# Performance work log

Measured on AMD Instinct MI355X. Metric: run time of the kernel, lower is better.

Reference implementation:

```python
import jax, jax.numpy as jnp
import numpy as np

DIM = 256
NUM_HEADS = 8
HEAD_DIM = DIM // NUM_HEADS


def _conv1x1(x, W, scale, bias):
    # 1x1 conv (bias=False) + eval-mode BN folded to per-channel scale/shift
    y = jnp.einsum('oc,bchw->bohw', W, x)
    return y * scale[None, :, None, None] + bias[None, :, None, None]


def setup_inputs() -> dict:
    key = jax.random.key(0)
    ks = jax.random.split(key, 16)
    B, H, W = 4, 64, 64
    Hu, Wu = 32, 32
    inp = {
        'x': jax.random.normal(ks[0], (B, DIM, H, W), jnp.float32),
        'upper_feat': jax.random.normal(ks[1], (B, DIM, Hu, Wu), jnp.float32),
        'Wq': jax.random.normal(ks[2], (DIM, DIM), jnp.float32) * 0.02,
        'q_scale': jax.random.uniform(ks[3], (DIM,), jnp.float32, 0.5, 1.5),
        'q_bias': jax.random.normal(ks[4], (DIM,), jnp.float32) * 0.02,
        'Wkv': jax.random.normal(ks[5], (2 * DIM, DIM), jnp.float32) * 0.02,
        'kv_scale': jax.random.uniform(ks[6], (2 * DIM,), jnp.float32, 0.5, 1.5),
        'kv_bias': jax.random.normal(ks[7], (2 * DIM,), jnp.float32) * 0.02,
        'Wpe': jax.random.normal(ks[8], (DIM, 1, 7, 7), jnp.float32) * 0.02,
        'pe_scale': jax.random.uniform(ks[9], (DIM,), jnp.float32, 0.5, 1.5),
        'pe_bias': jax.random.normal(ks[10], (DIM,), jnp.float32) * 0.02,
        'Wproj': jax.random.normal(ks[11], (DIM, DIM), jnp.float32) * 0.02,
        'proj_scale': jax.random.uniform(ks[12], (DIM,), jnp.float32, 0.5, 1.5),
        'proj_bias': jax.random.normal(ks[13], (DIM,), jnp.float32) * 0.02,
    }
    return inp


def reference(x, upper_feat, Wq, q_scale, q_bias, Wkv, kv_scale, kv_bias,
              Wpe, pe_scale, pe_bias, Wproj, proj_scale, proj_bias):
    B, C, H, W = x.shape
    N = H * W
    _, _, Hu, Wu = upper_feat.shape
    Nu = Hu * Wu

    # q branch: 1x1 conv+BN on x -> [B, heads, N, head_dim]
    q = _conv1x1(x, Wq, q_scale, q_bias)
    q = q.reshape(B, NUM_HEADS, HEAD_DIM, N).transpose(0, 1, 3, 2)

    # kv branch on upper (coarser) feature -> [B, heads, Nu, 2*head_dim]
    kv = _conv1x1(upper_feat, Wkv, kv_scale, kv_bias)
    kv = kv.reshape(B, NUM_HEADS, 2 * HEAD_DIM, Nu).transpose(0, 1, 3, 2)
    k, v = kv[..., :HEAD_DIM], kv[..., HEAD_DIM:]

    # cross attention: q over x pixels, k/v over upper pixels
    sim = jnp.einsum('bhnd,bhmd->bhnm', q, k) * (HEAD_DIM ** -0.5)
    attn = jax.nn.softmax(sim, axis=-1)
    ao = jnp.einsum('bhnm,bhmd->bhnd', attn, v)  # [B,h,N,hd]
    ao = ao.transpose(0, 1, 3, 2).reshape(B, C, H, W)

    # positional-encoding branch: depthwise 7x7 conv on v at upper resolution
    v_r = v.transpose(0, 1, 3, 2).reshape(B, C, Hu, Wu)
    v_pe = jax.lax.conv_general_dilated(
        v_r, Wpe, window_strides=(1, 1), padding=((3, 3), (3, 3)),
        feature_group_count=C,
        dimension_numbers=('NCHW', 'OIHW', 'NCHW'))
    v_pe = v_pe * pe_scale[None, :, None, None] + pe_bias[None, :, None, None]
    # bilinear upsample to x resolution (align_corners=False semantics)
    v_pe = jax.image.resize(v_pe, (B, C, H, W), method='bilinear')

    out = ao + v_pe
    return _conv1x1(out, Wproj, proj_scale, proj_bias)
```

## Files before the change

### kernel.cpp

```cpp
#include <hip/hip_runtime.h>
#include <hip/hip_bf16.h>

#define DIM 256
#define NHEADS 8
#define HDIM 32
#define Bq 4
#define Nq 4096
#define Nu 1024

typedef __attribute__((ext_vector_type(8))) short bf16x8;
typedef __attribute__((ext_vector_type(16))) float f32x16;
typedef __attribute__((ext_vector_type(4))) unsigned short us4;

__device__ __forceinline__ ushort f2bf(float x) {
    union { float f; unsigned u; } v; v.f = x;
    unsigned r = v.u + 0x7fffu + ((v.u >> 16) & 1u);
    return (ushort)(r >> 16);
}
__device__ __forceinline__ float bf2f(ushort u) {
    union { unsigned u; float f; } v; v.u = ((unsigned)u) << 16;
    return v.f;
}

__global__ __launch_bounds__(256) void prepro(
    const float* __restrict__ Wq, ushort* __restrict__ Oq,
    const float* __restrict__ Wkv, ushort* __restrict__ Okv,
    const float* __restrict__ Wp, ushort* __restrict__ Oph, ushort* __restrict__ Opl)
{
    const int i = blockIdx.x * 256 + threadIdx.x;
    if (i < 65536) {
        Oq[i] = f2bf(Wq[i]);
        float w = Wp[i];
        ushort h = f2bf(w);
        Oph[i] = h;
        Opl[i] = f2bf(w - bf2f(h));
    }
    Okv[i] = f2bf(Wkv[i]);
}

__global__ __launch_bounds__(256, 4) void qkv_mfma(
    const ushort* __restrict__ Wqb, const float* __restrict__ x,
    const float* __restrict__ q_scale, const float* __restrict__ q_bias, float qmult,
    const ushort* __restrict__ Wkvb, const float* __restrict__ upper,
    const float* __restrict__ kv_scale, const float* __restrict__ kv_bias,
    ushort* __restrict__ Qb, ushort* __restrict__ Kb, ushort* __restrict__ Vb)
{
    __shared__ __align__(16) ushort S[32 * 256];
    const int id = blockIdx.x;
    const int tid = threadIdx.x;

    const float* In; int N, n0, b, oh; bool isQ;
    if (id < 512) {
        isQ = true; In = x; N = 4096;
        n0 = (id & 127) * 32; b = id >> 7; oh = 0;
    } else {
        int q = id - 512;
        isQ = false; In = upper; N = 1024;
        n0 = (q & 31) * 32; oh = (q >> 5) & 1; b = q >> 6;
    }

    {
        const int n4 = (tid & 7) * 4, c8 = (tid >> 3) * 8;
        const float* ip = In + ((size_t)b * 256 + c8) * N + n0 + n4;
        unsigned ow[4][4];
        #pragma unroll
        for (int rp = 0; rp < 4; ++rp) {
            float4 f0 = *(const float4*)(ip + (size_t)(2 * rp) * N);
            float4 f1 = *(const float4*)(ip + (size_t)(2 * rp + 1) * N);
            asm("v_cvt_pk_bf16_f32 %0, %1, %2" : "=v"(ow[0][rp]) : "v"(f0.x), "v"(f1.x));
            asm("v_cvt_pk_bf16_f32 %0, %1, %2" : "=v"(ow[1][rp]) : "v"(f0.y), "v"(f1.y));
            asm("v_cvt_pk_bf16_f32 %0, %1, %2" : "=v"(ow[2][rp]) : "v"(f0.z), "v"(f1.z));
            asm("v_cvt_pk_bf16_f32 %0, %1, %2" : "=v"(ow[3][rp]) : "v"(f0.w), "v"(f1.w));
        }
        #pragma unroll
        for (int j = 0; j < 4; ++j) {
            const int n = n4 + j;
            const int slot = ((c8 >> 3) ^ (n & 15)) & 31;
            *(uint4*)(&S[n * 256 + (slot << 3)]) = *(const uint4*)&ow[j][0];
        }
    }
    __syncthreads();

    const int w = tid >> 6, l = tid & 63;
    const int l31 = l & 31, hi = l >> 5;
    const int nsw = l31 & 15;
    const ushort* Srow = &S[l31 * 256];

    if (isQ) {
        const ushort* w0 = Wqb + (size_t)(w * 64 + l31) * 256 + hi * 8;
        const ushort* w1 = w0 + (size_t)32 * 256;
        f32x16 acc0 = {}, acc1 = {};
        #pragma unroll 8
        for (int kk = 0; kk < 256; kk += 16) {
            const int slot = (((kk >> 3) + hi) ^ nsw) & 31;
            bf16x8 av = *(const bf16x8*)(Srow + (slot << 3));
            bf16x8 h0 = *(const bf16x8*)(w0 + kk);
            bf16x8 h1 = *(const bf16x8*)(w1 + kk);
            acc0 = __builtin_amdgcn_mfma_f32_32x32x16_bf16(av, h0, acc0, 0, 0, 0);
            acc1 = __builtin_amdgcn_mfma_f32_32x32x16_bf16(av, h1, acc1, 0, 0, 0);
        }
        #pragma unroll
        for (int t = 0; t < 2; ++t) {
            const f32x16 a = t ? acc1 : acc0;
            const int orow = w * 64 + t * 32 + l31;
            const float sc = q_scale[orow] * qmult;
            const float bi = q_bias[orow] * qmult;
            const int bh = b * 8 + 2 * w + t;
            ushort* Oa = Qb + ((size_t)bh * 4096) * 32 + l31;
            #pragma unroll
            for (int r = 0; r < 16; ++r) {
                const int dn = (r & 3) + 8 * (r >> 2) + 4 * hi;
                Oa[(size_t)(n0 + dn) * 32] = f2bf(a[r] * sc + bi);
            }
        }
    } else {
        const int h = oh * 4 + w;
        const ushort* wk = Wkvb + (size_t)(h * 64 + l31) * 256 + hi * 8;
        const ushort* wv = wk + (size_t)32 * 256;
        f32x16 accK = {}, accV = {};
        #pragma unroll 8
        for (int kk = 0; kk < 256; kk += 16) {
            const int slot = (((kk >> 3) + hi) ^ nsw) & 31;
            bf16x8 av = *(const bf16x8*)(Srow + (slot << 3));
            bf16x8 k0 = *(const bf16x8*)(wk + kk);
            bf16x8 v0 = *(const bf16x8*)(wv + kk);
            accK = __builtin_amdgcn_mfma_f32_32x32x16_bf16(av, k0, accK, 0, 0, 0);
            accV = __builtin_amdgcn_mfma_f32_32x32x16_bf16(v0, av, accV, 0, 0, 0);
        }
        const int bh = b * 8 + h;
        {
            const float sc = kv_scale[h * 64 + l31];
            const float bi = kv_bias[h * 64 + l31];
            ushort* Oa = Kb + ((size_t)bh * 1024) * 32 + l31;
            #pragma unroll
            for (int r = 0; r < 16; ++r) {
                const int dn = (r & 3) + 8 * (r >> 2) + 4 * hi;
                Oa[(size_t)(n0 + dn) * 32] = f2bf(accK[r] * sc + bi);
            }
        }
        {
            ushort* Ob = Vb + (size_t)bh * 32 * 1024;
            #pragma unroll
            for (int r = 0; r < 16; ++r) {
                const int dr = (r & 3) + 8 * (r >> 2) + 4 * hi;
                const float sc = kv_scale[h * 64 + 32 + dr];
                const float bi = kv_bias[h * 64 + 32 + dr];
                Ob[(size_t)dr * 1024 + n0 + l31] = f2bf(accV[r] * sc + bi);
            }
        }
    }
}

__global__ __launch_bounds__(256, 4) void attn_dw(
    const ushort* __restrict__ Qb, const ushort* __restrict__ Kt,
    const ushort* __restrict__ Vb, ushort* __restrict__ ao,
    const float* __restrict__ Wpe, const float* __restrict__ pe_scale,
    const float* __restrict__ pe_bias, ushort* __restrict__ vpe)
{
    __shared__ __align__(16) unsigned char smem[16384];
    const int tid = threadIdx.x;

    if (blockIdx.x < 1024) {
        const int w = tid >> 6, l = tid & 63;
        const int l31 = l & 31, hi = l >> 5;
        const int lid = blockIdx.x;
        const int j = lid >> 3;
        const int bh = (lid & 7) * 4 + (j >> 5);
        const int qbase = (j & 31) * 128 + w * 32;

        unsigned char (*ldsbuf)[8192] = (unsigned char(*)[8192])smem;

        const ushort* Qp = Qb + ((size_t)bh * 4096 + qbase) * 32;
        const unsigned char* Kg = (const unsigned char*)(Kt + (size_t)bh * 1024 * 32);
        const unsigned char* Vg = (const unsigned char*)(Vb + (size_t)bh * 32 * 1024);

        const bf16x8 qb0 = *(const bf16x8*)(Qp + (size_t)l31 * 32 + hi * 8);
        const bf16x8 qb1 = *(const bf16x8*)(Qp + (size_t)l31 * 32 + 16 + hi * 8);

        const int kr = tid >> 2, kc = tid & 3;
        const int vd = tid >> 3, vc = tid & 7;
        const int kwr = (kr * 64 + kc * 16) ^ ((kr & 7) << 4);
        const int vwr = vd * 128 + ((vc ^ (vd & 7)) << 4);

        f32x16 acc = {};
        float l_run = 0.f;

        uint4 kreg = *(const uint4*)(Kg + kr * 64 + kc * 16);
        uint4 vreg = *(const uint4*)(Vg + vd * 2048 + vc * 16);
        *(uint4*)(&ldsbuf[0][kwr]) = kreg;
        *(uint4*)(&ldsbuf[0][4096 + vwr]) = vreg;
        __syncthreads();

        for (int ph = 0; ph < 16; ++ph) {
            const int cur = ph & 1;
            if (ph < 15) {
                const size_t koff = (size_t)(ph + 1) * 4096;
                const int    voff = (ph + 1) * 128;
                kreg = *(const uint4*)(Kg + koff + kr * 64 + kc * 16);
                vreg = *(const uint4*)(Vg + (size_t)vd * 2048 + voff + vc * 16);
            }
            const unsigned char* Kl = &ldsbuf[cur][0];
            const unsigned char* Vl = &ldsbuf[cur][4096];

            #pragma unroll
            for (int s = 0; s < 2; ++s) {
                const int r = s * 32 + l31;
                bf16x8 ka0 = *(const bf16x8*)(Kl + ((r * 64 + hi * 16) ^ ((r & 7) << 4)));
                bf16x8 ka1 = *(const bf16x8*)(Kl + ((r * 64 + 32 + hi * 16) ^ ((r & 7) << 4)));
                bf16x8 va0 = *(const bf16x8*)(Vl + l31 * 128 + (((s * 4 + hi)     ^ (l31 & 7)) << 4));
                bf16x8 va1 = *(const bf16x8*)(Vl + l31 * 128 + (((s * 4 + 2 + hi) ^ (l31 & 7)) << 4));

                f32x16 sv = {};
                sv = __builtin_amdgcn_mfma_f32_32x32x16_bf16(ka0, qb0, sv, 0, 0, 0);
                sv = __builtin_amdgcn_mfma_f32_32x32x16_bf16(ka1, qb1, sv, 0, 0, 0);

                float p[16];
                #pragma unroll
                for (int r2 = 0; r2 < 16; ++r2) p[r2] = __builtin_amdgcn_exp2f(sv[r2]);
                l_run += (((p[0] + p[1]) + (p[2] + p[3])) + ((p[4] + p[5]) + (p[6] + p[7])))
                       + (((p[8] + p[9]) + (p[10] + p[11])) + ((p[12] + p[13]) + (p[14] + p[15])));

                int c[8];
                #pragma unroll
                for (int i = 0; i < 8; ++i)
                    asm("v_cvt_pk_bf16_f32 %0, %1, %2" : "=v"(c[i]) : "v"(p[2 * i]), "v"(p[2 * i + 1]));
                asm("v_permlane32_swap_b32 %0, %1" : "+v"(c[0]), "+v"(c[2]));
                asm("v_permlane32_swap_b32 %0, %1" : "+v"(c[1]), "+v"(c[3]));
                asm("v_permlane32_swap_b32 %0, %1" : "+v"(c[4]), "+v"(c[6]));
                asm("v_permlane32_swap_b32 %0, %1" : "+v"(c[5]), "+v"(c[7]));

                union { int i[4]; bf16x8 v; } b0u, b1u;
                b0u.i[0] = c[0]; b0u.i[1] = c[1]; b0u.i[2] = c[2]; b0u.i[3] = c[3];
                b1u.i[0] = c[4]; b1u.i[1] = c[5]; b1u.i[2] = c[6]; b1u.i[3] = c[7];

                acc = __builtin_amdgcn_mfma_f32_32x32x16_bf16(va0, b0u.v, acc, 0, 0, 0);
                acc = __builtin_amdgcn_mfma_f32_32x32x16_bf16(va1, b1u.v, acc, 0, 0, 0);
            }

            if (ph < 15) {
                const int nxt = cur ^ 1;
                *(uint4*)(&ldsbuf[nxt][kwr]) = kreg;
                *(uint4*)(&ldsbuf[nxt][4096 + vwr]) = vreg;
            }
            __syncthreads();
        }

        l_run += __shfl_xor(l_run, 32);
        float inv = 1.0f / l_run;

        ushort* aob = ao + ((size_t)(bh >> 3) * 256 + (bh & 7) * 32) * 4096 + qbase + l31;
        #pragma unroll
        for (int r = 0; r < 16; ++r) {
            const int d = (r & 3) + 8 * (r >> 2) + 4 * hi;
            aob[(size_t)d * 4096] = f2bf(acc[r] * inv);
        }
    } else {
        const int bc = blockIdx.x - 1024;
        const int b = bc >> 8, c = bc & 255;
        const ushort* vp = Vb + ((size_t)(b * 8 + (c >> 5)) * 32 + (c & 31)) * 1024;

        float* t   = (float*)smem;
        float* v32 = (float*)(smem + 5776);
        float* wl  = (float*)(smem + 9872);

        for (int i = tid; i < 38 * 38; i += 256) {
            int yy = i / 38 - 3, xx = i % 38 - 3;
            t[i] = (yy >= 0 && yy < 32 && xx >= 0 && xx < 32) ? bf2f(vp[yy * 32 + xx]) : 0.f;
        }
        if (tid < 49) wl[tid] = Wpe[(size_t)c * 49 + tid];
        __syncthreads();

        const float sc = pe_scale[c], bi = pe_bias[c];
        for (int i = tid; i < 1024; i += 256) {
            int y = i >> 5, x = i & 31;
            float s = 0.f;
            #pragma unroll
            for (int ky = 0; ky < 7; ++ky)
                #pragma unroll
                for (int kx = 0; kx < 7; ++kx)
                    s += t[(y + ky) * 38 + x + kx] * wl[ky * 7 + kx];
            v32[i] = s * sc + bi;
        }
        __syncthreads();

        ushort* op = vpe + (size_t)bc * 4096;
        #pragma unroll
        for (int p = 0; p < 16; ++p) {
            int idx = p * 256 + tid;
            int x = idx & 63, y = idx >> 6;
            float cx = x * 0.5f - 0.25f;
            float cy = y * 0.5f - 0.25f;
            int x0 = (x - 1) >> 1, y0 = (y - 1) >> 1;
            float fx = cx - x0, fy = cy - y0;
            int x0c = max(x0, 0), x1c = min(x0 + 1, 31);
            int y0c = max(y0, 0), y1c = min(y0 + 1, 31);
            float v00 = v32[y0c * 32 + x0c], v01 = v32[y0c * 32 + x1c];
            float v10 = v32[y1c * 32 + x0c], v11 = v32[y1c * 32 + x1c];
            float val = (1.f - fy) * ((1.f - fx) * v00 + fx * v01)
                      + fy * ((1.f - fx) * v10 + fx * v11);
            op[idx] = f2bf(val);
        }
    }
}

__global__ __launch_bounds__(512, 2) void proj_mfma(
    const ushort* __restrict__ Whi, const ushort* __restrict__ Wlo,
    const ushort* __restrict__ ao, const ushort* __restrict__ vpe,
    const float* __restrict__ scale, const float* __restrict__ bias,
    float* __restrict__ Out)
{
    __shared__ __align__(16) ushort S[64 * 256];
    const int tid = threadIdx.x;
    const int b  = blockIdx.z;
    const int n0 = blockIdx.x * 64;

    {
        const int n4 = (tid & 15) * 4;
        const int c8 = (tid >> 4) * 8;
        const ushort* ap = ao  + ((size_t)b * 256 + c8) * 4096 + n0 + n4;
        const ushort* vp = vpe + ((size_t)b * 256 + c8) * 4096 + n0 + n4;
        unsigned ow[4][4];
        #pragma unroll
        for (int rp = 0; rp < 4; ++rp) {
            uint2 a0 = *(const uint2*)(ap + (size_t)(2 * rp) * 4096);
            uint2 a1 = *(const uint2*)(ap + (size_t)(2 * rp + 1) * 4096);
            uint2 v0 = *(const uint2*)(vp + (size_t)(2 * rp) * 4096);
            uint2 v1 = *(const uint2*)(vp + (size_t)(2 * rp + 1) * 4096);
            const unsigned a0u[2] = { a0.x, a0.y };
            const unsigned a1u[2] = { a1.x, a1.y };
            const unsigned v0u[2] = { v0.x, v0.y };
            const unsigned v1u[2] = { v1.x, v1.y };
            #pragma unroll
            for (int q = 0; q < 2; ++q) {
                float s0lo = __uint_as_float(a0u[q] << 16)
                           + __uint_as_float(v0u[q] << 16);
                float s0hi = __uint_as_float(a0u[q] & 0xffff0000u)
                           + __uint_as_float(v0u[q] & 0xffff0000u);
                float s1lo = __uint_as_float(a1u[q] << 16)
                           + __uint_as_float(v1u[q] << 16);
                float s1hi = __uint_as_float(a1u[q] & 0xffff0000u)
                           + __uint_as_float(v1u[q] & 0xffff0000u);
                unsigned plo, phi;
                asm("v_cvt_pk_bf16_f32 %0, %1, %2" : "=v"(plo) : "v"(s0lo), "v"(s1lo));
                asm("v_cvt_pk_bf16_f32 %0, %1, %2" : "=v"(phi) : "v"(s0hi), "v"(s1hi));
                ow[2 * q][rp]     = plo;
                ow[2 * q + 1][rp] = phi;
            }
        }
        #pragma unroll
        for (int j = 0; j < 4; ++j) {
            const int n = n4 + j;
            const int slot = (((c8 >> 3) ^ (n & 15)) & 31);
            *(uint4*)(&S[n * 256 + (slot << 3)]) = *(const uint4*)&ow[j][0];
        }
    }
    __syncthreads();

    const int w = tid >> 6, l = tid & 63;
    const int l31 = l & 31, hi = l >> 5;
    const int wo = w & 3, wn = w >> 2;
    const int ob = wo * 64;

    const ushort* wh0 = Whi + (size_t)(ob + l31) * 256 + hi * 8;
    const ushort* wh1 = wh0 + (size_t)32 * 256;
    const ushort* wl0 = Wlo + (size_t)(ob + l31) * 256 + hi * 8;
    const ushort* wl1 = wl0 + (size_t)32 * 256;

    const int nloc = wn * 32 + l31;
    const ushort* Srow = &S[nloc * 256];
    const int nsw = nloc & 15;

    f32x16 acc0 = {}, acc1 = {};
    #pragma unroll 4
    for (int kk = 0; kk < 256; kk += 16) {
        const int slot = (((kk >> 3) + hi) ^ nsw) & 31;
        bf16x8 av = *(const bf16x8*)(Srow + (slot << 3));
        bf16x8 h0 = *(const bf16x8*)(wh0 + kk);
        bf16x8 h1 = *(const bf16x8*)(wh1 + kk);
        bf16x8 g0 = *(const bf16x8*)(wl0 + kk);
        bf16x8 g1 = *(const bf16x8*)(wl1 + kk);
        acc0 = __builtin_amdgcn_mfma_f32_32x32x16_bf16(h0, av, acc0, 0, 0, 0);
        acc1 = __builtin_amdgcn_mfma_f32_32x32x16_bf16(h1, av, acc1, 0, 0, 0);
        acc0 = __builtin_amdgcn_mfma_f32_32x32x16_bf16(g0, av, acc0, 0, 0, 0);
        acc1 = __builtin_amdgcn_mfma_f32_32x32x16_bf16(g1, av, acc1, 0, 0, 0);
    }

    float* Ob = Out + (size_t)b * 256 * 4096 + n0 + wn * 32 + l31;
    #pragma unroll
    for (int r = 0; r < 16; ++r) {
        const int dr = (r & 3) + 8 * (r >> 2) + 4 * hi;
        const int oA = ob + dr, oB = ob + 32 + dr;
        Ob[(size_t)oA * 4096] = acc0[r] * scale[oA] + bias[oA];
        Ob[(size_t)oB * 4096] = acc1[r] * scale[oB] + bias[oB];
    }
}

extern "C" void kernel_launch(void* const* d_in, const int* in_sizes, int n_in,
                              void* d_out, int out_size, void* d_ws, size_t ws_size,
                              hipStream_t stream)
{
    const float* x        = (const float*)d_in[0];
    const float* upper    = (const float*)d_in[1];
    const float* Wq       = (const float*)d_in[2];
    const float* q_scale  = (const float*)d_in[3];
    const float* q_bias   = (const float*)d_in[4];
    const float* Wkv      = (const float*)d_in[5];
    const float* kv_scale = (const float*)d_in[6];
    const float* kv_bias  = (const float*)d_in[7];
    const float* Wpe      = (const float*)d_in[8];
    const float* pe_scale = (const float*)d_in[9];
    const float* pe_bias  = (const float*)d_in[10];
    const float* Wproj    = (const float*)d_in[11];
    const float* proj_scale = (const float*)d_in[12];
    const float* proj_bias  = (const float*)d_in[13];
    float* out = (float*)d_out;

    ushort* Qb   = (ushort*)d_ws;
    ushort* Kb   = Qb + (size_t)32 * 4096 * 32;
    ushort* Vb   = Kb + (size_t)32 * 1024 * 32;
    ushort* ao   = Vb + (size_t)32 * 1024 * 32;
    ushort* vpe  = ao + (size_t)Bq * DIM * Nq;
    ushort* Wqb  = vpe + (size_t)Bq * DIM * Nq;
    ushort* Wkvb = Wqb + 256 * 256;
    ushort* Wph  = Wkvb + 512 * 256;
    ushort* Wpl  = Wph + 256 * 256;

    const float qmult = 0.17677669529663687f * 1.4426950408889634f;

    prepro<<<dim3(512), 256, 0, stream>>>(Wq, Wqb, Wkv, Wkvb, Wproj, Wph, Wpl);

    qkv_mfma<<<dim3(768), 256, 0, stream>>>(Wqb, x, q_scale, q_bias, qmult,
                                            Wkvb, upper, kv_scale, kv_bias,
                                            Qb, Kb, Vb);

    attn_dw<<<dim3(2048), 256, 0, stream>>>(Qb, Kb, Vb, ao,
                                            Wpe, pe_scale, pe_bias, vpe);

    proj_mfma<<<dim3(64, 1, 4), 512, 0, stream>>>(Wph, Wpl, ao, vpe,
                                                  proj_scale, proj_bias, out);
}
```

Before: 81.78 us.

## Fuse bilinear upsample of positional encoding into projection kernel prologue

The depthwise conv branch now writes the low-resolution fp32 result (32x32 per channel) to global memory, and the bilinear 2x upsample is done inside the projection kernel while it stages its input tile. This avoids writing and rereading a full-resolution bf16 vpe tensor. The projection prologue gains extra gather loads and arithmetic, with neighbouring pixels reread from L2, and the added value is no longer rounded to bf16 before summation.

```diff
diff --git a/kernel.cpp b/kernel.cpp
--- a/kernel.cpp
+++ b/kernel.cpp
@@ -19,6 +19,10 @@
 }
 __device__ __forceinline__ float bf2f(ushort u) {
     union { unsigned u; float f; } v; v.u = ((unsigned)u) << 16;
+    return v.f;
+}
+__device__ __forceinline__ float bfu2f(unsigned lo16shifted) {
+    union { unsigned u; float f; } v; v.u = lo16shifted;
     return v.f;
 }
 
@@ -155,7 +159,7 @@
     const ushort* __restrict__ Qb, const ushort* __restrict__ Kt,
     const ushort* __restrict__ Vb, ushort* __restrict__ ao,
     const float* __restrict__ Wpe, const float* __restrict__ pe_scale,
-    const float* __restrict__ pe_bias, ushort* __restrict__ vpe)
+    const float* __restrict__ pe_bias, float* __restrict__ v32f)
 {
     __shared__ __align__(16) unsigned char smem[16384];
     const int tid = threadIdx.x;
@@ -259,9 +263,8 @@
         const int b = bc >> 8, c = bc & 255;
         const ushort* vp = Vb + ((size_t)(b * 8 + (c >> 5)) * 32 + (c & 31)) * 1024;
 
-        float* t   = (float*)smem;
-        float* v32 = (float*)(smem + 5776);
-        float* wl  = (float*)(smem + 9872);
+        float* t  = (float*)smem;
+        float* wl = (float*)(smem + 5776);
 
         for (int i = tid; i < 38 * 38; i += 256) {
             int yy = i / 38 - 3, xx = i % 38 - 3;
@@ -271,6 +274,7 @@
         __syncthreads();
 
         const float sc = pe_scale[c], bi = pe_bias[c];
+        float* op = v32f + (size_t)bc * 1024;
         for (int i = tid; i < 1024; i += 256) {
             int y = i >> 5, x = i & 31;
             float s = 0.f;
@@ -279,79 +283,82 @@
                 #pragma unroll
                 for (int kx = 0; kx < 7; ++kx)
                     s += t[(y + ky) * 38 + x + kx] * wl[ky * 7 + kx];
-            v32[i] = s * sc + bi;
-        }
-        __syncthreads();
-
-        ushort* op = vpe + (size_t)bc * 4096;
-        #pragma unroll
-        for (int p = 0; p < 16; ++p) {
-            int idx = p * 256 + tid;
-            int x = idx & 63, y = idx >> 6;
-            float cx = x * 0.5f - 0.25f;
-            float cy = y * 0.5f - 0.25f;
-            int x0 = (x - 1) >> 1, y0 = (y - 1) >> 1;
-            float fx = cx - x0, fy = cy - y0;
-            int x0c = max(x0, 0), x1c = min(x0 + 1, 31);
-            int y0c = max(y0, 0), y1c = min(y0 + 1, 31);
-            float v00 = v32[y0c * 32 + x0c], v01 = v32[y0c * 32 + x1c];
-            float v10 = v32[y1c * 32 + x0c], v11 = v32[y1c * 32 + x1c];
-            float val = (1.f - fy) * ((1.f - fx) * v00 + fx * v01)
-                      + fy * ((1.f - fx) * v10 + fx * v11);
-            op[idx] = f2bf(val);
+            op[i] = s * sc + bi;
         }
     }
 }
 
 __global__ __launch_bounds__(512, 2) void proj_mfma(
     const ushort* __restrict__ Whi, const ushort* __restrict__ Wlo,
-    const ushort* __restrict__ ao, const ushort* __restrict__ vpe,
+    const ushort* __restrict__ ao, const float* __restrict__ v32f,
     const float* __restrict__ scale, const float* __restrict__ bias,
     float* __restrict__ Out)
 {
     __shared__ __align__(16) ushort S[64 * 256];
     const int tid = threadIdx.x;
     const int b  = blockIdx.z;
-    const int n0 = blockIdx.x * 64;
+    const int y  = blockIdx.x;
+    const int n0 = y * 64;
 
     {
-        const int n4 = (tid & 15) * 4;
+        const int m  = tid & 15;
         const int c8 = (tid >> 4) * 8;
-        const ushort* ap = ao  + ((size_t)b * 256 + c8) * 4096 + n0 + n4;
-        const ushort* vp = vpe + ((size_t)b * 256 + c8) * 4096 + n0 + n4;
-        unsigned ow[4][4];
-        #pragma unroll
-        for (int rp = 0; rp < 4; ++rp) {
-            uint2 a0 = *(const uint2*)(ap + (size_t)(2 * rp) * 4096);
-            uint2 a1 = *(const uint2*)(ap + (size_t)(2 * rp + 1) * 4096);
-            uint2 v0 = *(const uint2*)(vp + (size_t)(2 * rp) * 4096);
-            uint2 v1 = *(const uint2*)(vp + (size_t)(2 * rp + 1) * 4096);
-            const unsigned a0u[2] = { a0.x, a0.y };
-            const unsigned a1u[2] = { a1.x, a1.y };
-            const unsigned v0u[2] = { v0.x, v0.y };
-            const unsigned v1u[2] = { v1.x, v1.y };
-            #pragma unroll
-            for (int q = 0; q < 2; ++q) {
-                float s0lo = __uint_as_float(a0u[q] << 16)
-                           + __uint_as_float(v0u[q] << 16);
-                float s0hi = __uint_as_float(a0u[q] & 0xffff0000u)
-                           + __uint_as_float(v0u[q] & 0xffff0000u);
-                float s1lo = __uint_as_float(a1u[q] << 16)
-                           + __uint_as_float(v1u[q] << 16);
-                float s1hi = __uint_as_float(a1u[q] & 0xffff0000u)
-                           + __uint_as_float(v1u[q] & 0xffff0000u);
-                unsigned plo, phi;
-                asm("v_cvt_pk_bf16_f32 %0, %1, %2" : "=v"(plo) : "v"(s0lo), "v"(s1lo));
-                asm("v_cvt_pk_bf16_f32 %0, %1, %2" : "=v"(phi) : "v"(s0hi), "v"(s1hi));
-                ow[2 * q][rp]     = plo;
-                ow[2 * q + 1][rp] = phi;
-            }
-        }
+
+        const int y0  = (y - 1) >> 1;
+        const float fy = (y & 1) ? 0.25f : 0.75f;
+        const float gy = 1.0f - fy;
+        const int y0c = max(y0, 0), y1c = min(y0 + 1, 31);
+        const int aIdx = max(m - 1, 0), cIdx = min(m + 1, 15);
+
+        float sval[4][8];
+        #pragma unroll
+        for (int cc = 0; cc < 8; ++cc) {
+            const int ch = c8 + cc;
+            const float* rowb = v32f + (size_t)(b * 256 + ch) * 1024;
+            const float* rT = rowb + y0c * 32;
+            const float* rB = rowb + y1c * 32;
+            float2 ta = *(const float2*)(rT + 2 * aIdx);
+            float2 tb = *(const float2*)(rT + 2 * m);
+            float2 tc = *(const float2*)(rT + 2 * cIdx);
+            float2 ba = *(const float2*)(rB + 2 * aIdx);
+            float2 bb = *(const float2*)(rB + 2 * m);
+            float2 bc2 = *(const float2*)(rB + 2 * cIdx);
+            const float t_m1 = (m == 0)  ? tb.x : ta.y;
+            const float t_p2 = (m == 15) ? tb.y : tc.x;
+            const float b_m1 = (m == 0)  ? bb.x : ba.y;
+            const float b_p2 = (m == 15) ? bb.y : bc2.x;
+            const float ht0 = 0.25f * t_m1 + 0.75f * tb.x;
+            const float ht1 = 0.75f * tb.x + 0.25f * tb.y;
+            const float ht2 = 0.25f * tb.x + 0.75f * tb.y;
+            const float ht3 = 0.75f * tb.y + 0.25f * t_p2;
+            const float hb0 = 0.25f * b_m1 + 0.75f * bb.x;
+            const float hb1 = 0.75f * bb.x + 0.25f * bb.y;
+            const float hb2 = 0.25f * bb.x + 0.75f * bb.y;
+            const float hb3 = 0.75f * bb.y + 0.25f * b_p2;
+
+            const ushort* ap = ao + (size_t)(b * 256 + ch) * 4096 + n0 + m * 4;
+            uint2 av = *(const uint2*)ap;
+            const float a0 = bfu2f(av.x << 16);
+            const float a1 = bfu2f(av.x & 0xffff0000u);
+            const float a2 = bfu2f(av.y << 16);
+            const float a3 = bfu2f(av.y & 0xffff0000u);
+
+            sval[0][cc] = a0 + (gy * ht0 + fy * hb0);
+            sval[1][cc] = a1 + (gy * ht1 + fy * hb1);
+            sval[2][cc] = a2 + (gy * ht2 + fy * hb2);
+            sval[3][cc] = a3 + (gy * ht3 + fy * hb3);
+        }
+
         #pragma unroll
         for (int j = 0; j < 4; ++j) {
-            const int n = n4 + j;
+            unsigned ow[4];
+            #pragma unroll
+            for (int rp = 0; rp < 4; ++rp)
+                asm("v_cvt_pk_bf16_f32 %0, %1, %2"
+                    : "=v"(ow[rp]) : "v"(sval[j][2 * rp]), "v"(sval[j][2 * rp + 1]));
+            const int n = m * 4 + j;
             const int slot = (((c8 >> 3) ^ (n & 15)) & 31);
-            *(uint4*)(&S[n * 256 + (slot << 3)]) = *(const uint4*)&ow[j][0];
+            *(uint4*)(&S[n * 256 + (slot << 3)]) = *(const uint4*)&ow[0];
         }
     }
     __syncthreads();
@@ -419,8 +426,8 @@
     ushort* Kb   = Qb + (size_t)32 * 4096 * 32;
     ushort* Vb   = Kb + (size_t)32 * 1024 * 32;
     ushort* ao   = Vb + (size_t)32 * 1024 * 32;
-    ushort* vpe  = ao + (size_t)Bq * DIM * Nq;
-    ushort* Wqb  = vpe + (size_t)Bq * DIM * Nq;
+    float*  v32f = (float*)(ao + (size_t)Bq * DIM * Nq);
+    ushort* Wqb  = (ushort*)(v32f + (size_t)Bq * DIM * Nu);
     ushort* Wkvb = Wqb + 256 * 256;
     ushort* Wph  = Wkvb + 512 * 256;
     ushort* Wpl  = Wph + 256 * 256;
@@ -434,8 +441,8 @@
                                             Qb, Kb, Vb);
 
     attn_dw<<<dim3(2048), 256, 0, stream>>>(Qb, Kb, Vb, ao,
-                                            Wpe, pe_scale, pe_bias, vpe);
-
-    proj_mfma<<<dim3(64, 1, 4), 512, 0, stream>>>(Wph, Wpl, ao, vpe,
+                                            Wpe, pe_scale, pe_bias, v32f);
+
+    proj_mfma<<<dim3(64, 1, 4), 512, 0, stream>>>(Wph, Wpl, ao, v32f,
                                                   proj_scale, proj_bias, out);
 }
```

Result: faster. 78.83 us, median of 2 (-3.6%).
